# Kernel optimization log

Hardware: AMD Instinct MI355X
Metric: run time of the kernel (lower is better)

The kernel has to match this reference:

```python
import jax, jax.numpy as jnp
import numpy as np

B, S, D = 2, 2048, 1024
H, KH = 16, 4            # query heads, kv heads
DK = D // H              # 64
REP = H // KH            # queries per kv head


def _rope(x):
    # x: (B, h, S, dk); non-interleaved rotate-half RoPE as in source
    dk = x.shape[-1]
    half = dk // 2
    seq = x.shape[2]
    theta = 10000.0 ** (-(jnp.arange(half, dtype=jnp.float32) / half))
    pos = jnp.arange(seq, dtype=jnp.float32)
    freqs = pos[:, None] * theta[None, :]          # (S, half)
    cos = jnp.cos(freqs)[None, None]               # (1,1,S,half)
    sin = jnp.sin(freqs)[None, None]
    x1, x2 = x[..., :half], x[..., half:]
    return jnp.concatenate([x1 * cos - x2 * sin, x2 * cos + x1 * sin], axis=-1)


def setup_inputs() -> dict:
    key = jax.random.key(0)
    ks = jax.random.split(key, 9)
    sd = 1.0 / np.sqrt(D)
    x = jax.random.normal(ks[0], (B, S, D), dtype=jnp.float32)
    # causal mask: 1 where attend allowed, 0 where masked (mask==0 -> -inf)
    mask = jnp.tril(jnp.ones((S, S), dtype=jnp.int32))[None, None]
    Wq = jax.random.normal(ks[1], (D, H * DK), dtype=jnp.float32) * sd
    bq = jnp.zeros((H * DK,), dtype=jnp.float32)
    Wk = jax.random.normal(ks[2], (D, KH * DK), dtype=jnp.float32) * sd
    bk = jnp.zeros((KH * DK,), dtype=jnp.float32)
    Wv = jax.random.normal(ks[3], (D, KH * DK), dtype=jnp.float32) * sd
    bv = jnp.zeros((KH * DK,), dtype=jnp.float32)
    Wo = jax.random.normal(ks[4], (H * DK, D), dtype=jnp.float32) * sd
    bo = jnp.zeros((D,), dtype=jnp.float32)
    return {"x": x, "mask": mask, "Wq": Wq, "bq": bq, "Wk": Wk, "bk": bk,
            "Wv": Wv, "bv": bv, "Wo": Wo, "bo": bo}


def reference(x, mask, Wq, bq, Wk, bk, Wv, bv, Wo, bo):
    b, s, _ = x.shape
    q = (x @ Wq + bq).reshape(b, s, H, DK).transpose(0, 2, 1, 3)   # (B,H,S,DK)
    k = (x @ Wk + bk).reshape(b, s, KH, DK).transpose(0, 2, 1, 3)  # (B,KH,S,DK)
    v = (x @ Wv + bv).reshape(b, s, KH, DK).transpose(0, 2, 1, 3)
    q = _rope(q)
    k = _rope(k)
    k = jnp.repeat(k, REP, axis=1)  # GQA expand: (B,H,S,DK)
    v = jnp.repeat(v, REP, axis=1)
    attn = jnp.einsum('bhqd,bhkd->bhqk', q, k) / np.sqrt(DK).astype(np.float32)
    attn = jnp.where(mask == 0, -jnp.inf, attn)
    score = jax.nn.softmax(attn, axis=-1)
    out = jnp.einsum('bhqk,bhkd->bhqd', score, v)   # (B,H,S,DK)
    out = out.transpose(0, 2, 1, 3).reshape(b, s, H * DK)
    return out @ Wo + bo
```

## Files before the change

kernel.cpp:

```cpp
#include <hip/hip_runtime.h>
#include <math.h>

#define B_   2
#define S_   2048
#define D_   1024
#define H_   16
#define KH_  4
#define DK_  64

using bf16x8 = __attribute__((ext_vector_type(8))) short;
using bf16x4 = __attribute__((ext_vector_type(4))) short;
using f32x4  = __attribute__((ext_vector_type(4))) float;
using u32x4  = __attribute__((ext_vector_type(4))) unsigned int;
using u32x2  = __attribute__((ext_vector_type(2))) unsigned int;

__device__ inline unsigned short f2bf(float f) {
    unsigned u = __float_as_uint(f);
    u += 0x7FFFu + ((u >> 16) & 1u);
    return (unsigned short)(u >> 16);
}
__device__ inline float bf2f(unsigned short u) {
    return __uint_as_float(((unsigned)u) << 16);
}

#ifdef __has_builtin
#if __has_builtin(__builtin_amdgcn_cvt_pk_bf16_f32)
#define PKBF16 1
#endif
#if __has_builtin(__builtin_amdgcn_exp2f)
#define NEXP2 1
#endif
#endif
__device__ inline unsigned pk2bf(float a, float b) {
#ifdef PKBF16
    auto r = __builtin_amdgcn_cvt_pk_bf16_f32(a, b);
    unsigned u; __builtin_memcpy(&u, &r, 4);
    return u;
#else
    return (unsigned)f2bf(a) | ((unsigned)f2bf(b) << 16);
#endif
}
__device__ inline float fexp2(float x) {
#ifdef NEXP2
    return __builtin_amdgcn_exp2f(x);
#else
    return exp2f(x);
#endif
}

#define GL16(gp, lp) __builtin_amdgcn_global_load_lds( \
    (const __attribute__((address_space(1))) unsigned int*)(gp), \
    (__attribute__((address_space(3))) unsigned int*)(lp), 16, 0, 0)

__global__ __launch_bounds__(256) void prep_kernel(
    const float* __restrict__ x,
    const float* __restrict__ Wq, const float* __restrict__ Wk,
    const float* __restrict__ Wv, const float* __restrict__ Wo,
    unsigned short* __restrict__ xb,
    unsigned short* __restrict__ WqkvT,
    unsigned short* __restrict__ WoT)
{
    __shared__ float T[64][65];
    const int t = threadIdx.x;
    int bx = blockIdx.x;

    if (bx < 2048) {
        const int i = bx * 256 + t;
        f32x4 a = *(const f32x4*)(x + (long)i * 8);
        f32x4 b = *(const f32x4*)(x + (long)i * 8 + 4);
        bf16x8 o;
        o[0] = (short)f2bf(a[0]); o[1] = (short)f2bf(a[1]);
        o[2] = (short)f2bf(a[2]); o[3] = (short)f2bf(a[3]);
        o[4] = (short)f2bf(b[0]); o[5] = (short)f2bf(b[1]);
        o[6] = (short)f2bf(b[2]); o[7] = (short)f2bf(b[3]);
        *(bf16x8*)(xb + (long)i * 8) = o;
        return;
    }
    bx -= 2048;
    const float* in; unsigned short* out; int C;
    if (bx < 256)      { in = Wq; out = WqkvT;               C = 1024; }
    else if (bx < 320) { in = Wk; out = WqkvT + 1024 * 1024; C = 256;  bx -= 256; }
    else if (bx < 384) { in = Wv; out = WqkvT + 1280 * 1024; C = 256;  bx -= 320; }
    else               { in = Wo; out = WoT;                 C = 1024; bx -= 384; }
    const int R  = 1024, nr = 16;
    const int r0 = (bx % nr) * 64;
    const int c0 = (bx / nr) * 64;
    {
        const int r  = t >> 2;
        const int cq = (t & 3) * 16;
        const float* src = in + (long)(r0 + r) * C + c0 + cq;
        #pragma unroll
        for (int i = 0; i < 4; ++i) {
            f32x4 v = *(const f32x4*)(src + i * 4);
            T[r][cq + i * 4 + 0] = v[0];
            T[r][cq + i * 4 + 1] = v[1];
            T[r][cq + i * 4 + 2] = v[2];
            T[r][cq + i * 4 + 3] = v[3];
        }
    }
    __syncthreads();
    {
        const int c  = t >> 2;
        const int rq = (t & 3) * 16;
        bf16x8 p0, p1;
        #pragma unroll
        for (int i = 0; i < 8; ++i) {
            p0[i] = (short)f2bf(T[rq + i][c]);
            p1[i] = (short)f2bf(T[rq + 8 + i][c]);
        }
        unsigned short* dst = out + (long)(c0 + c) * R + r0 + rq;
        *(bf16x8*)dst       = p0;
        *(bf16x8*)(dst + 8) = p1;
    }
}

template<bool BF16OUT>
__global__ __launch_bounds__(256) void gemm64_kernel(
    const unsigned short* __restrict__ A,
    const unsigned short* __restrict__ Bt,
    const float* __restrict__ b0,
    const float* __restrict__ b1,
    const float* __restrict__ b2,
    float* __restrict__ outf,
    unsigned short* __restrict__ outb,
    int N, int K)
{
    __shared__ unsigned short As[2][64][32];
    __shared__ unsigned short Bs[2][128][32];

    const int t  = threadIdx.x;
    const int m0 = blockIdx.x * 64;
    const int n0 = blockIdx.y * 128;

    const int w    = t >> 6;
    const int lane = t & 63;
    const int n    = lane & 15;
    const int quad = lane >> 4;
    const int wm   = (w >> 1) * 32;
    const int wn   = (w & 1) * 64;

    const int lr4 = lane >> 2;
    const int cs  = ((lane & 3) ^ (lr4 & 3)) * 8;

    const unsigned short* gA  = A  + (long)(m0 + w * 16 + lr4) * K + cs;
    const unsigned short* gB0 = Bt + (long)(n0 + w * 32 + lr4) * K + cs;
    const unsigned short* gB1 = gB0 + (long)16 * K;

    GL16(gA,  &As[0][w * 16][0]);
    GL16(gB0, &Bs[0][w * 32][0]);
    GL16(gB1, &Bs[0][w * 32 + 16][0]);

    f32x4 acc[2][4];
    #pragma unroll
    for (int i = 0; i < 2; ++i)
        #pragma unroll
        for (int j = 0; j < 4; ++j) acc[i][j] = 0.0f;

    const int cr = (quad ^ (n & 3)) * 8;

    for (int k0 = 0; k0 < K; k0 += 32) {
        const int cur = (k0 >> 5) & 1;
        __syncthreads();
        if (k0 + 32 < K) {
            const int nb = cur ^ 1;
            GL16(gA  + k0 + 32, &As[nb][w * 16][0]);
            GL16(gB0 + k0 + 32, &Bs[nb][w * 32][0]);
            GL16(gB1 + k0 + 32, &Bs[nb][w * 32 + 16][0]);
        }

        bf16x8 af[2], bfr[4];
        #pragma unroll
        for (int i = 0; i < 2; ++i)
            af[i] = *(const bf16x8*)&As[cur][wm + i * 16 + n][cr];
        #pragma unroll
        for (int j = 0; j < 4; ++j)
            bfr[j] = *(const bf16x8*)&Bs[cur][wn + j * 16 + n][cr];
        #pragma unroll
        for (int mi = 0; mi < 2; ++mi)
            #pragma unroll
            for (int ni = 0; ni < 4; ++ni)
                acc[mi][ni] = __builtin_amdgcn_mfma_f32_16x16x32_bf16(
                    af[mi], bfr[ni], acc[mi][ni], 0, 0, 0);
    }

    #pragma unroll
    for (int mi = 0; mi < 2; ++mi) {
        #pragma unroll
        for (int r = 0; r < 4; ++r) {
            const int gm = m0 + wm + mi * 16 + quad * 4 + r;
            #pragma unroll
            for (int ni = 0; ni < 4; ++ni) {
                const int gn = n0 + wn + ni * 16 + n;
                if (BF16OUT) {
                    const float b = (gn < 1024) ? b0[gn]
                                  : (gn < 1280) ? b1[gn - 1024]
                                                : b2[gn - 1280];
                    outb[(long)gm * N + gn] = f2bf(acc[mi][ni][r] + b);
                } else {
                    outf[(long)gm * N + gn] = acc[mi][ni][r] + b0[gn];
                }
            }
        }
    }
}

__global__ __launch_bounds__(256) void scatter_kernel(
    const unsigned short* __restrict__ qkvm,
    unsigned short* __restrict__ qbuf,
    unsigned short* __restrict__ kbuf,
    unsigned short* __restrict__ vbuf)
{
    __shared__ unsigned short T[64][72];
    const int t = threadIdx.x;
    int bx = blockIdx.x;

    if (bx < 1280) {
        const int idx = bx * 256 + t;
        const int m   = idx / 80;
        const int rem = idx - m * 80;
        const int h20 = rem >> 2;
        const int d0  = (rem & 3) * 8;

        const int s  = m & (S_ - 1);
        const int bb = m >> 11;
        const int col0 = (h20 < 16) ? h20 * 64 + d0 : 1024 + (h20 - 16) * 64 + d0;
        const float scl = (h20 < 16) ? 0.1803368801111606f : 1.0f;

        const bf16x8 x1v = *(const bf16x8*)(qkvm + (long)m * 1536 + col0);
        const bf16x8 x2v = *(const bf16x8*)(qkvm + (long)m * 1536 + col0 + 32);
        bf16x8 o1, o2;
        #pragma unroll
        for (int j = 0; j < 8; ++j) {
            const int d = d0 + j;
            const float theta = exp2f(-(float)d * (13.287712379549449f / 32.0f));
            const float f = (float)s * theta;
            const float c = cosf(f) * scl, sn = sinf(f) * scl;
            const float x1 = bf2f((unsigned short)x1v[j]);
            const float x2 = bf2f((unsigned short)x2v[j]);
            o1[j] = (short)f2bf(x1 * c - x2 * sn);
            o2[j] = (short)f2bf(x2 * c + x1 * sn);
        }
        unsigned short* dst = (h20 < 16)
            ? qbuf + ((long)(bb * H_ + h20) * S_ + s) * DK_ + d0
            : kbuf + ((long)(bb * KH_ + (h20 - 16)) * S_ + s) * DK_ + d0;
        *(bf16x8*)dst        = o1;
        *(bf16x8*)(dst + 32) = o2;
        return;
    }
    bx -= 1280;
    const int bkh = bx >> 5;
    const int s0  = (bx & 31) * 64;
    {
        const int s  = t >> 2;
        const int dq = (t & 3) * 16;
        const unsigned short* src =
            qkvm + (long)((bkh >> 2) * S_ + s0 + s) * 1536 + 1280 + (bkh & 3) * 64 + dq;
        *(bf16x8*)&T[s][dq]     = *(const bf16x8*)src;
        *(bf16x8*)&T[s][dq + 8] = *(const bf16x8*)(src + 8);
    }
    __syncthreads();
    {
        const int d  = t >> 2;
        const int sq = (t & 3) * 16;
        bf16x8 p0, p1;
        #pragma unroll
        for (int i = 0; i < 8; ++i) {
            p0[i] = (short)T[sq + i][d];
            p1[i] = (short)T[sq + 8 + i][d];
        }
        unsigned short* dst = vbuf + ((long)bkh * DK_ + d) * S_ + s0 + sq;
        *(bf16x8*)dst       = p0;
        *(bf16x8*)(dst + 8) = p1;
    }
}

__global__ __launch_bounds__(256) void attn_kernel(
    const unsigned short* __restrict__ qb,
    const unsigned short* __restrict__ kbf,
    const unsigned short* __restrict__ vT,
    unsigned short* __restrict__ ot)
{
    __shared__ __align__(16) unsigned short Ks[2][64][64];
    __shared__ __align__(16) unsigned short Vs[2][64][64];
    __shared__ __align__(16) unsigned short Ps[4][16][64];

    const int tid = threadIdx.x;
    const int bx  = blockIdx.x;
    const int qt  = 31 - (bx >> 5);
    const int bh  = bx & 31;
    const int b   = bh >> 4, h = bh & 15;
    const int kh  = h >> 2;
    const int q0  = qt * 64;

    const int wv   = tid >> 6;
    const int lane = tid & 63;
    const int n    = lane & 15;
    const int quad = lane >> 4;
    const int xk   = n & 7;

    const unsigned short* qp =
        qb + ((long)(b * H_ + h) * S_ + q0 + wv * 16 + n) * DK_;
    const bf16x8 qa0 = *(const bf16x8*)(qp + quad * 8);
    const bf16x8 qa1 = *(const bf16x8*)(qp + 32 + quad * 8);

    f32x4 O[4];
    #pragma unroll
    for (int dt = 0; dt < 4; ++dt) O[dt] = 0.0f;
    float lsum = 0.f;

    const unsigned short* kbase = kbf + (long)(b * KH_ + kh) * S_ * DK_;
    const unsigned short* vbase = vT  + (long)(b * KH_ + kh) * DK_ * S_;

    const int ntiles = qt + 1;
    const int srow = tid >> 3;
    const int lc   = tid & 7;
    const int sc8  = lc * 8;
    const int pcs  = (lc ^ (srow & 7)) * 8;

    u32x4 kr0 = *(const u32x4*)(kbase + (long)srow * DK_ + sc8);
    u32x4 kr1 = *(const u32x4*)(kbase + (long)(32 + srow) * DK_ + sc8);
    u32x4 vr0 = *(const u32x4*)(vbase + (long)srow * S_ + sc8);
    u32x4 vr1 = *(const u32x4*)(vbase + (long)(32 + srow) * S_ + sc8);
    *(u32x4*)&Ks[0][srow][pcs]      = kr0;
    *(u32x4*)&Ks[0][32 + srow][pcs] = kr1;
    *(u32x4*)&Vs[0][srow][pcs]      = vr0;
    *(u32x4*)&Vs[0][32 + srow][pcs] = vr1;

    for (int u = 0; u < ntiles; ++u) {
        const int cur = u & 1;
        const int kb  = u * 64;
        __syncthreads();

        if (u + 1 < ntiles) {
            const int kbn = kb + 64;
            kr0 = *(const u32x4*)(kbase + (long)(kbn + srow) * DK_ + sc8);
            kr1 = *(const u32x4*)(kbase + (long)(kbn + 32 + srow) * DK_ + sc8);
            vr0 = *(const u32x4*)(vbase + (long)srow * S_ + kbn + sc8);
            vr1 = *(const u32x4*)(vbase + (long)(32 + srow) * S_ + kbn + sc8);
        }

        f32x4 sc[4];
        #pragma unroll
        for (int ct = 0; ct < 4; ++ct) {
            const bf16x8 kf0 =
                *(const bf16x8*)&Ks[cur][ct * 16 + n][(quad ^ xk) * 8];
            const bf16x8 kf1 =
                *(const bf16x8*)&Ks[cur][ct * 16 + n][((quad + 4) ^ xk) * 8];
            f32x4 c = 0.0f;
            c = __builtin_amdgcn_mfma_f32_16x16x32_bf16(kf0, qa0, c, 0, 0, 0);
            c = __builtin_amdgcn_mfma_f32_16x16x32_bf16(kf1, qa1, c, 0, 0, 0);
            sc[ct] = c;
        }

        if (u == qt) {
            const int qg = q0 + wv * 16 + n;
            #pragma unroll
            for (int ct = 0; ct < 4; ++ct) {
                const int kq = kb + ct * 16 + quad * 4;
                #pragma unroll
                for (int r = 0; r < 4; ++r)
                    if (kq + r > qg) sc[ct][r] = -INFINITY;
            }
        }
        f32x4 rs4 = 0.0f;
        #pragma unroll
        for (int ct = 0; ct < 4; ++ct) {
            #pragma unroll
            for (int r = 0; r < 4; ++r) {
                const float p = fexp2(sc[ct][r]);
                sc[ct][r] = p;
                rs4[r] += p;
            }
        }
        lsum += (rs4[0] + rs4[1]) + (rs4[2] + rs4[3]);

        #pragma unroll
        for (int ct = 0; ct < 4; ++ct) {
            u32x2 pw;
            pw[0] = pk2bf(sc[ct][0], sc[ct][1]);
            pw[1] = pk2bf(sc[ct][2], sc[ct][3]);
            const int pc = ((2 * ct + (quad >> 1)) ^ xk) * 8 + (quad & 1) * 4;
            *(u32x2*)&Ps[wv][n][pc] = pw;
        }
        const bf16x8 pb0 = *(const bf16x8*)&Ps[wv][n][(quad ^ xk) * 8];
        const bf16x8 pb1 = *(const bf16x8*)&Ps[wv][n][((quad + 4) ^ xk) * 8];

        #pragma unroll
        for (int dt = 0; dt < 4; ++dt) {
            const bf16x8 av0 =
                *(const bf16x8*)&Vs[cur][dt * 16 + n][(quad ^ xk) * 8];
            const bf16x8 av1 =
                *(const bf16x8*)&Vs[cur][dt * 16 + n][((quad + 4) ^ xk) * 8];
            O[dt] = __builtin_amdgcn_mfma_f32_16x16x32_bf16(av0, pb0, O[dt], 0, 0, 0);
            O[dt] = __builtin_amdgcn_mfma_f32_16x16x32_bf16(av1, pb1, O[dt], 0, 0, 0);
        }

        if (u + 1 < ntiles) {
            const int nb = cur ^ 1;
            *(u32x4*)&Ks[nb][srow][pcs]      = kr0;
            *(u32x4*)&Ks[nb][32 + srow][pcs] = kr1;
            *(u32x4*)&Vs[nb][srow][pcs]      = vr0;
            *(u32x4*)&Vs[nb][32 + srow][pcs] = vr1;
        }
    }

    lsum += __shfl_xor(lsum, 16);
    lsum += __shfl_xor(lsum, 32);
    const float inv = 1.0f / lsum;
    #pragma unroll
    for (int dt = 0; dt < 4; ++dt) {
        u32x2 pw;
        pw[0] = pk2bf(O[dt][0] * inv, O[dt][1] * inv);
        pw[1] = pk2bf(O[dt][2] * inv, O[dt][3] * inv);
        const int pc = ((2 * dt + (quad >> 1)) ^ xk) * 8 + (quad & 1) * 4;
        *(u32x2*)&Ps[wv][n][pc] = pw;
    }
    const int fr = lane >> 3;
    const int c8l = lane & 7;
    #pragma unroll
    for (int it = 0; it < 2; ++it) {
        const int row = it * 8 + fr;
        const int q   = q0 + wv * 16 + row;
        unsigned short* op = ot + ((long)(b * S_ + q) * H_ + h) * DK_ + c8l * 8;
        *(bf16x8*)op = *(const bf16x8*)&Ps[wv][row][(c8l ^ fr) * 8];
    }
}

extern "C" void kernel_launch(void* const* d_in, const int* in_sizes, int n_in,
                              void* d_out, int out_size, void* d_ws, size_t ws_size,
                              hipStream_t stream)
{
    const float* x  = (const float*)d_in[0];
    const float* Wq = (const float*)d_in[2];
    const float* bq = (const float*)d_in[3];
    const float* Wk = (const float*)d_in[4];
    const float* bk = (const float*)d_in[5];
    const float* Wv = (const float*)d_in[6];
    const float* bv = (const float*)d_in[7];
    const float* Wo = (const float*)d_in[8];
    const float* bo = (const float*)d_in[9];
    float* out = (float*)d_out;

    unsigned short* ws    = (unsigned short*)d_ws;
    unsigned short* xb    = ws;
    unsigned short* qkvm  = xb + 4194304;
    unsigned short* qbuf  = qkvm + 6291456;
    unsigned short* kbuf  = qbuf + 4194304;
    unsigned short* vbuf  = kbuf + 1048576;
    unsigned short* WqkvT = vbuf + 1048576;
    unsigned short* WoT   = WqkvT + 1572864;
    unsigned short* ob    = qkvm;

    prep_kernel<<<2688, 256, 0, stream>>>(x, Wq, Wk, Wv, Wo, xb, WqkvT, WoT);

    gemm64_kernel<true><<<dim3(64, 12), 256, 0, stream>>>(
        xb, WqkvT, bq, bk, bv, nullptr, qkvm, 1536, 1024);

    scatter_kernel<<<1536, 256, 0, stream>>>(qkvm, qbuf, kbuf, vbuf);

    attn_kernel<<<B_ * H_ * (S_ / 64), 256, 0, stream>>>(qbuf, kbuf, vbuf, ob);

    gemm64_kernel<false><<<dim3(64, 8), 256, 0, stream>>>(
        ob, WoT, bo, nullptr, nullptr, out, nullptr, 1024, 1024);
}
```

Baseline: 189.6 us.

## Process 128 query rows per attention block to reuse K/V tiles

The attention kernel now covers 128 query rows per block instead of 64. Each wave handles two 16-row halves, sharing every K and V fragment it reads from shared memory across both halves, and the grid is halved to 512 blocks. Block order is remapped so the longest causal tiles are scheduled first. This cuts K/V global and LDS traffic per query and adds MFMA work per LDS read, at the cost of more registers per thread, fewer resident blocks and coarser load balancing.

```diff
diff --git a/kernel.cpp b/kernel.cpp
--- a/kernel.cpp
+++ b/kernel.cpp
@@ -286,11 +286,12 @@
 
     const int tid = threadIdx.x;
     const int bx  = blockIdx.x;
-    const int qt  = 31 - (bx >> 5);
+    const int g   = bx >> 5;
+    const int a   = (g < 8) ? (15 - g) : (g - 8);
     const int bh  = bx & 31;
     const int b   = bh >> 4, h = bh & 15;
     const int kh  = h >> 2;
-    const int q0  = qt * 64;
+    const int q0  = a * 128;
 
     const int wv   = tid >> 6;
     const int lane = tid & 63;
@@ -299,19 +300,24 @@
     const int xk   = n & 7;
 
     const unsigned short* qp =
-        qb + ((long)(b * H_ + h) * S_ + q0 + wv * 16 + n) * DK_;
-    const bf16x8 qa0 = *(const bf16x8*)(qp + quad * 8);
-    const bf16x8 qa1 = *(const bf16x8*)(qp + 32 + quad * 8);
-
-    f32x4 O[4];
+        qb + ((long)(b * H_ + h) * S_ + q0 + wv * 32 + n) * DK_;
+    bf16x8 qa[2][2];
+    qa[0][0] = *(const bf16x8*)(qp + quad * 8);
+    qa[0][1] = *(const bf16x8*)(qp + 32 + quad * 8);
+    qa[1][0] = *(const bf16x8*)(qp + 16 * DK_ + quad * 8);
+    qa[1][1] = *(const bf16x8*)(qp + 16 * DK_ + 32 + quad * 8);
+
+    f32x4 O[2][4];
     #pragma unroll
-    for (int dt = 0; dt < 4; ++dt) O[dt] = 0.0f;
-    float lsum = 0.f;
+    for (int hf = 0; hf < 2; ++hf)
+        #pragma unroll
+        for (int dt = 0; dt < 4; ++dt) O[hf][dt] = 0.0f;
+    float ls0 = 0.f, ls1 = 0.f;
 
     const unsigned short* kbase = kbf + (long)(b * KH_ + kh) * S_ * DK_;
     const unsigned short* vbase = vT  + (long)(b * KH_ + kh) * DK_ * S_;
 
-    const int ntiles = qt + 1;
+    const int ntiles = 2 * a + 2;
     const int srow = tid >> 3;
     const int lc   = tid & 7;
     const int sc8  = lc * 8;
@@ -339,46 +345,66 @@
             vr1 = *(const u32x4*)(vbase + (long)(32 + srow) * S_ + kbn + sc8);
         }
 
-        f32x4 sc[4];
+        f32x4 s0[4], s1[4];
         #pragma unroll
         for (int ct = 0; ct < 4; ++ct) {
             const bf16x8 kf0 =
                 *(const bf16x8*)&Ks[cur][ct * 16 + n][(quad ^ xk) * 8];
             const bf16x8 kf1 =
                 *(const bf16x8*)&Ks[cur][ct * 16 + n][((quad + 4) ^ xk) * 8];
-            f32x4 c = 0.0f;
-            c = __builtin_amdgcn_mfma_f32_16x16x32_bf16(kf0, qa0, c, 0, 0, 0);
-            c = __builtin_amdgcn_mfma_f32_16x16x32_bf16(kf1, qa1, c, 0, 0, 0);
-            sc[ct] = c;
-        }
-
-        if (u == qt) {
-            const int qg = q0 + wv * 16 + n;
+            f32x4 c0 = 0.0f, c1 = 0.0f;
+            c0 = __builtin_amdgcn_mfma_f32_16x16x32_bf16(kf0, qa[0][0], c0, 0, 0, 0);
+            c0 = __builtin_amdgcn_mfma_f32_16x16x32_bf16(kf1, qa[0][1], c0, 0, 0, 0);
+            c1 = __builtin_amdgcn_mfma_f32_16x16x32_bf16(kf0, qa[1][0], c1, 0, 0, 0);
+            c1 = __builtin_amdgcn_mfma_f32_16x16x32_bf16(kf1, qa[1][1], c1, 0, 0, 0);
+            s0[ct] = c0;
+            s1[ct] = c1;
+        }
+
+        if (u + 2 >= ntiles) {
+            const int qg0 = q0 + wv * 32 + n;
+            const int qg1 = qg0 + 16;
             #pragma unroll
             for (int ct = 0; ct < 4; ++ct) {
                 const int kq = kb + ct * 16 + quad * 4;
                 #pragma unroll
-                for (int r = 0; r < 4; ++r)
-                    if (kq + r > qg) sc[ct][r] = -INFINITY;
+                for (int r = 0; r < 4; ++r) {
+                    if (kq + r > qg0) s0[ct][r] = -INFINITY;
+                    if (kq + r > qg1) s1[ct][r] = -INFINITY;
+                }
             }
         }
-        f32x4 rs4 = 0.0f;
+
+        f32x4 ra = 0.0f, rb = 0.0f;
         #pragma unroll
         for (int ct = 0; ct < 4; ++ct) {
             #pragma unroll
             for (int r = 0; r < 4; ++r) {
-                const float p = fexp2(sc[ct][r]);
-                sc[ct][r] = p;
-                rs4[r] += p;
+                const float p0 = fexp2(s0[ct][r]);
+                const float p1 = fexp2(s1[ct][r]);
+                s0[ct][r] = p0; ra[r] += p0;
+                s1[ct][r] = p1; rb[r] += p1;
             }
         }
-        lsum += (rs4[0] + rs4[1]) + (rs4[2] + rs4[3]);
+        ls0 += (ra[0] + ra[1]) + (ra[2] + ra[3]);
+        ls1 += (rb[0] + rb[1]) + (rb[2] + rb[3]);
 
         #pragma unroll
         for (int ct = 0; ct < 4; ++ct) {
             u32x2 pw;
-            pw[0] = pk2bf(sc[ct][0], sc[ct][1]);
-            pw[1] = pk2bf(sc[ct][2], sc[ct][3]);
+            pw[0] = pk2bf(s0[ct][0], s0[ct][1]);
+            pw[1] = pk2bf(s0[ct][2], s0[ct][3]);
+            const int pc = ((2 * ct + (quad >> 1)) ^ xk) * 8 + (quad & 1) * 4;
+            *(u32x2*)&Ps[wv][n][pc] = pw;
+        }
+        const bf16x8 pa0 = *(const bf16x8*)&Ps[wv][n][(quad ^ xk) * 8];
+        const bf16x8 pa1 = *(const bf16x8*)&Ps[wv][n][((quad + 4) ^ xk) * 8];
+
+        #pragma unroll
+        for (int ct = 0; ct < 4; ++ct) {
+            u32x2 pw;
+            pw[0] = pk2bf(s1[ct][0], s1[ct][1]);
+            pw[1] = pk2bf(s1[ct][2], s1[ct][3]);
             const int pc = ((2 * ct + (quad >> 1)) ^ xk) * 8 + (quad & 1) * 4;
             *(u32x2*)&Ps[wv][n][pc] = pw;
         }
@@ -391,8 +417,10 @@
                 *(const bf16x8*)&Vs[cur][dt * 16 + n][(quad ^ xk) * 8];
             const bf16x8 av1 =
                 *(const bf16x8*)&Vs[cur][dt * 16 + n][((quad + 4) ^ xk) * 8];
-            O[dt] = __builtin_amdgcn_mfma_f32_16x16x32_bf16(av0, pb0, O[dt], 0, 0, 0);
-            O[dt] = __builtin_amdgcn_mfma_f32_16x16x32_bf16(av1, pb1, O[dt], 0, 0, 0);
+            O[0][dt] = __builtin_amdgcn_mfma_f32_16x16x32_bf16(av0, pa0, O[0][dt], 0, 0, 0);
+            O[0][dt] = __builtin_amdgcn_mfma_f32_16x16x32_bf16(av1, pa1, O[0][dt], 0, 0, 0);
+            O[1][dt] = __builtin_amdgcn_mfma_f32_16x16x32_bf16(av0, pb0, O[1][dt], 0, 0, 0);
+            O[1][dt] = __builtin_amdgcn_mfma_f32_16x16x32_bf16(av1, pb1, O[1][dt], 0, 0, 0);
         }
 
         if (u + 1 < ntiles) {
@@ -404,25 +432,31 @@
         }
     }
 
-    lsum += __shfl_xor(lsum, 16);
-    lsum += __shfl_xor(lsum, 32);
-    const float inv = 1.0f / lsum;
-    #pragma unroll
-    for (int dt = 0; dt < 4; ++dt) {
-        u32x2 pw;
-        pw[0] = pk2bf(O[dt][0] * inv, O[dt][1] * inv);
-        pw[1] = pk2bf(O[dt][2] * inv, O[dt][3] * inv);
-        const int pc = ((2 * dt + (quad >> 1)) ^ xk) * 8 + (quad & 1) * 4;
-        *(u32x2*)&Ps[wv][n][pc] = pw;
-    }
-    const int fr = lane >> 3;
+    ls0 += __shfl_xor(ls0, 16);
+    ls0 += __shfl_xor(ls0, 32);
+    ls1 += __shfl_xor(ls1, 16);
+    ls1 += __shfl_xor(ls1, 32);
+    const int fr  = lane >> 3;
     const int c8l = lane & 7;
     #pragma unroll
-    for (int it = 0; it < 2; ++it) {
-        const int row = it * 8 + fr;
-        const int q   = q0 + wv * 16 + row;
-        unsigned short* op = ot + ((long)(b * S_ + q) * H_ + h) * DK_ + c8l * 8;
-        *(bf16x8*)op = *(const bf16x8*)&Ps[wv][row][(c8l ^ fr) * 8];
+    for (int hf = 0; hf < 2; ++hf) {
+        const float inv = 1.0f / (hf ? ls1 : ls0);
+        #pragma unroll
+        for (int dt = 0; dt < 4; ++dt) {
+            u32x2 pw;
+            pw[0] = pk2bf(O[hf][dt][0] * inv, O[hf][dt][1] * inv);
+            pw[1] = pk2bf(O[hf][dt][2] * inv, O[hf][dt][3] * inv);
+            const int pc = ((2 * dt + (quad >> 1)) ^ xk) * 8 + (quad & 1) * 4;
+            *(u32x2*)&Ps[wv][n][pc] = pw;
+        }
+        #pragma unroll
+        for (int it = 0; it < 2; ++it) {
+            const int row = it * 8 + fr;
+            const int q   = q0 + wv * 32 + hf * 16 + row;
+            unsigned short* op =
+                ot + ((long)(b * S_ + q) * H_ + h) * DK_ + c8l * 8;
+            *(bf16x8*)op = *(const bf16x8*)&Ps[wv][row][(c8l ^ fr) * 8];
+        }
     }
 }
 
@@ -458,7 +492,7 @@
 
     scatter_kernel<<<1536, 256, 0, stream>>>(qkvm, qbuf, kbuf, vbuf);
 
-    attn_kernel<<<B_ * H_ * (S_ / 64), 256, 0, stream>>>(qbuf, kbuf, vbuf, ob);
+    attn_kernel<<<512, 256, 0, stream>>>(qbuf, kbuf, vbuf, ob);
 
     gemm64_kernel<false><<<dim3(64, 8), 256, 0, stream>>>(
         ob, WoT, bo, nullptr, nullptr, out, nullptr, 1024, 1024);
```

Measured after the change: 201.9 us. 1.06x slower.
